# Kernel tuning notes

Measured on AMD Instinct MI355X. Metric: run time of the kernel, lower is better.

The kernel has to match this reference:

```python
import jax, jax.numpy as jnp
import numpy as np

DIM, DEPTH, MULT = 512, 3, 4
E = 2 ** DEPTH            # 8 experts
HID = MULT * DIM          # 2048
B, S = 4, 1024


def setup_inputs() -> dict:
    key = jax.random.key(0)
    ks = jax.random.split(key, 7)
    sd = 1.0 / np.sqrt(DIM)
    sh = 1.0 / np.sqrt(HID)
    return {
        "x": jax.random.normal(ks[0], (B, S, DIM), dtype=jnp.float32),
        "rw": jax.random.normal(ks[1], (E - 1, DIM), dtype=jnp.float32) * sd,
        "rb": jax.random.normal(ks[2], (E - 1,), dtype=jnp.float32) * sd,
        "w1": jax.random.normal(ks[3], (E, DIM, HID), dtype=jnp.float32) * sd,
        "b1": jax.random.normal(ks[4], (E, HID), dtype=jnp.float32) * sd,
        "w2": jax.random.normal(ks[5], (E, HID, DIM), dtype=jnp.float32) * sh,
        "b2": jax.random.normal(ks[6], (E, DIM), dtype=jnp.float32) * sh,
    }


def _leaf_probs(flat_x, rw, rb):
    # Binary-tree soft routing: level d has 2**d routers at offset 2**d - 1.
    n_tok = flat_x.shape[0]
    leaf = jnp.ones((n_tok, 1), dtype=flat_x.dtype)
    for d in range(DEPTH):
        off, n = 2 ** d - 1, 2 ** d
        logits = flat_x @ rw[off:off + n].T + rb[off:off + n]   # [N, n]
        p = jax.nn.sigmoid(logits)
        # child probs: left = 1-p, right = p
        leaf = (leaf[:, :, None] * jnp.stack([1.0 - p, p], axis=2)).reshape(n_tok, 2 * n)
    return leaf  # [N, E]


def reference(x, rw, rb, w1, b1, w2, b2):
    b, s, dim = x.shape
    flat_x = x.reshape(b * s, dim)                               # [N, D]
    leaf_probs = _leaf_probs(flat_x, rw, rb)                     # [N, E]
    # Dense evaluation of all experts (soft-routing training path).
    h = jnp.einsum('nd,edh->neh', flat_x, w1) + b1[None]         # [N, E, H]
    h = jax.nn.gelu(h, approximate=False)                        # torch nn.GELU (erf)
    y = jnp.einsum('neh,ehd->ned', h, w2) + b2[None]             # [N, E, D]
    out = jnp.einsum('ned,ne->nd', y, leaf_probs)                # [N, D]
    return out.reshape(b, s, dim)
```

## Files before the change

kernel.cpp:

```cpp
#include <hip/hip_runtime.h>
#include <hip/hip_bf16.h>
#include <hip/hip_fp16.h>

#define DIM 512
#define HID 2048
#define NE 8
#define NTOK 4096

typedef _Float16 v8h __attribute__((ext_vector_type(8)));
typedef float v16f __attribute__((ext_vector_type(16)));

__device__ __forceinline__ void load16(const void* g, void* l) {
  __builtin_amdgcn_global_load_lds(
      (const __attribute__((address_space(1))) unsigned int*)g,
      (__attribute__((address_space(3))) unsigned int*)l, 16, 0, 0);
}

__device__ __forceinline__ float gelu_fast(float v) {
  float v2 = v * v;
  float u = v * __builtin_fmaf(0.07135481627f, v2, 1.5957691216f);
  float t = __expf(-u);
  return v * __builtin_amdgcn_rcpf(1.0f + t);
}

__global__ __launch_bounds__(256) void pre_kernel(const float* __restrict__ x,
                                                  const float* __restrict__ rw,
                                                  const float* __restrict__ rb,
                                                  const float* __restrict__ b2,
                                                  const float* __restrict__ w1,
                                                  const float* __restrict__ w2,
                                                  float* __restrict__ leaf,
                                                  _Float16* __restrict__ xh,
                                                  float* __restrict__ out,
                                                  _Float16* __restrict__ w1t,
                                                  _Float16* __restrict__ w2t) {
  __shared__ float tile[32][65];
  if (blockIdx.x < 1024) {
    const int lane = threadIdx.x & 63;
    const int wave = threadIdx.x >> 6;
    const int n = (blockIdx.x << 2) + wave;
    const float4* xv = (const float4*)(x + (size_t)n * DIM);
    const float4 x0 = xv[lane * 2], x1 = xv[lane * 2 + 1];
    v8h o;
    o[0] = (_Float16)x0.x; o[1] = (_Float16)x0.y; o[2] = (_Float16)x0.z; o[3] = (_Float16)x0.w;
    o[4] = (_Float16)x1.x; o[5] = (_Float16)x1.y; o[6] = (_Float16)x1.z; o[7] = (_Float16)x1.w;
    *(v8h*)(xh + (size_t)n * DIM + lane * 8) = o;
    float logits[7];
#pragma unroll
    for (int rr = 0; rr < 7; ++rr) {
      const float4* wv = (const float4*)(rw + rr * DIM);
      const float4 w0 = wv[lane * 2], w1v = wv[lane * 2 + 1];
      float s = x0.x * w0.x + x0.y * w0.y + x0.z * w0.z + x0.w * w0.w +
                x1.x * w1v.x + x1.y * w1v.y + x1.z * w1v.z + x1.w * w1v.w;
#pragma unroll
      for (int o2 = 32; o2; o2 >>= 1) s += __shfl_xor(s, o2, 64);
      logits[rr] = s + rb[rr];
    }
    const int eidx = lane & 7;
    const float p0 = 1.f / (1.f + __expf(-logits[0]));
    float f = ((eidx >> 2) & 1) ? p0 : 1.f - p0;
    const float p1 = 1.f / (1.f + __expf(-logits[1 + (eidx >> 2)]));
    f *= ((eidx >> 1) & 1) ? p1 : 1.f - p1;
    const float p2 = 1.f / (1.f + __expf(-logits[3 + (eidx >> 1)]));
    f *= (eidx & 1) ? p2 : 1.f - p2;
    if (lane < NE) leaf[(size_t)n * NE + lane] = f;
    float le[NE];
#pragma unroll
    for (int e = 0; e < NE; ++e) le[e] = __shfl(f, e, 64);
    float4 a0 = {0.f, 0.f, 0.f, 0.f}, a1 = {0.f, 0.f, 0.f, 0.f};
#pragma unroll
    for (int e = 0; e < NE; ++e) {
      const float4* bv = (const float4*)(b2 + (size_t)e * DIM + lane * 8);
      const float4 u0 = bv[0], u1 = bv[1];
      a0.x += le[e] * u0.x; a0.y += le[e] * u0.y; a0.z += le[e] * u0.z; a0.w += le[e] * u0.w;
      a1.x += le[e] * u1.x; a1.y += le[e] * u1.y; a1.z += le[e] * u1.z; a1.w += le[e] * u1.w;
    }
    float4* op = (float4*)(out + (size_t)n * DIM + lane * 8);
    op[0] = a0; op[1] = a1;
  } else {
    int bx = blockIdx.x - 1024;
    const float* in;
    _Float16* outp;
    int R, C;
    if (bx < 4096) { in = w1; outp = w1t; R = DIM; C = HID; }
    else { bx -= 4096; in = w2; outp = w2t; R = HID; C = DIM; }
    const int e = bx >> 9;
    const int rem = bx & 511;
    const int tiles_r = R >> 6;
    const int rt = rem % tiles_r;
    const int ct = rem / tiles_r;
    const int r0 = rt << 6, c0 = ct << 5;
    const size_t ebase = (size_t)e * R * C;
    const int tid = threadIdx.x;
#pragma unroll
    for (int it = 0; it < 2; ++it) {
      const int s = tid + (it << 8);
      const int row = s >> 3, cq = s & 7;
      const float4 v = *(const float4*)(in + ebase + (size_t)(r0 + row) * C + c0 + (cq << 2));
      tile[(cq << 2) + 0][row] = v.x;
      tile[(cq << 2) + 1][row] = v.y;
      tile[(cq << 2) + 2][row] = v.z;
      tile[(cq << 2) + 3][row] = v.w;
    }
    __syncthreads();
    const int c = tid >> 3, seg = tid & 7;
    v8h hv;
#pragma unroll
    for (int u = 0; u < 8; ++u) hv[u] = (_Float16)tile[c][(seg << 3) + u];
    *(v8h*)(outp + ebase + (size_t)(c0 + c) * R + r0 + (seg << 3)) = hv;
  }
}

__global__ __launch_bounds__(256, 2) void gemm1_kernel(const _Float16* __restrict__ xh,
                                                       const _Float16* __restrict__ w1t,
                                                       const float* __restrict__ b1,
                                                       const float* __restrict__ leaf,
                                                       _Float16* __restrict__ H) {
  const int bx = blockIdx.x;
  const int e = bx & 7;
  const int t = bx >> 3;
  const int mt = t & 15;
  const int nt = t >> 4;
  const int m0 = mt << 8, n0 = nt << 7;

  __shared__ alignas(16) _Float16 As[256 * 64];
  __shared__ alignas(16) _Float16 Bs[128 * 64];

  const int tid = threadIdx.x;
  const int lane = tid & 63;
  const int wave = tid >> 6;
  const int wm = wave >> 1, wn = wave & 1;
  const int c = lane & 31, h2 = lane >> 5;
  const int cx = c & 7;

  const int strow = tid >> 3;
  const int c8 = (tid & 7) ^ (strow & 7);
  const _Float16* pa[8];
  const _Float16* pb[4];
  _Float16* la[8];
  _Float16* lb[4];
#pragma unroll
  for (int i = 0; i < 8; ++i) {
    pa[i] = xh + (size_t)(m0 + strow + 32 * i) * DIM + (c8 << 3);
    la[i] = As + tid * 8 + i * 2048;
  }
#pragma unroll
  for (int i = 0; i < 4; ++i) {
    pb[i] = w1t + ((size_t)e * HID + n0 + strow + 32 * i) * DIM + (c8 << 3);
    lb[i] = Bs + tid * 8 + i * 2048;
  }
  const _Float16* fA[4];
  const _Float16* fB[2];
#pragma unroll
  for (int i = 0; i < 4; ++i) fA[i] = As + ((wm << 7) + (i << 5) + c) * 64;
#pragma unroll
  for (int j = 0; j < 2; ++j) fB[j] = Bs + ((wn << 6) + (j << 5) + c) * 64;

  v16f acc[4][2];
#pragma unroll
  for (int i = 0; i < 4; ++i)
#pragma unroll
    for (int j = 0; j < 2; ++j)
      acc[i][j] = v16f{0.f,0.f,0.f,0.f,0.f,0.f,0.f,0.f,0.f,0.f,0.f,0.f,0.f,0.f,0.f,0.f};

#pragma unroll
  for (int kk = 0; kk < 8; ++kk) {
#pragma unroll
    for (int i = 0; i < 8; ++i) load16(pa[i] + kk * 64, la[i]);
#pragma unroll
    for (int i = 0; i < 4; ++i) load16(pb[i] + kk * 64, lb[i]);
    __syncthreads();
#pragma unroll
    for (int ks = 0; ks < 4; ++ks) {
      const int so = ((((ks << 1) + h2) ^ cx) << 3);
      v8h a[4], b[2];
#pragma unroll
      for (int i = 0; i < 4; ++i) a[i] = *(const v8h*)(fA[i] + so);
#pragma unroll
      for (int j = 0; j < 2; ++j) b[j] = *(const v8h*)(fB[j] + so);
#pragma unroll
      for (int i = 0; i < 4; ++i)
#pragma unroll
        for (int j = 0; j < 2; ++j)
          acc[i][j] = __builtin_amdgcn_mfma_f32_32x32x16_f16(a[i], b[j], acc[i][j], 0, 0, 0);
    }
    __syncthreads();
  }

  const float* b1e = b1 + (size_t)e * HID;
  _Float16* He = H + (size_t)e * NTOK * HID;
  const int colb = n0 + (wn << 6) + c;
  const float bias0 = b1e[colb];
  const float bias1 = b1e[colb + 32];
#pragma unroll
  for (int i = 0; i < 4; ++i) {
    const int rb0 = m0 + (wm << 7) + (i << 5) + (h2 << 2);
#pragma unroll
    for (int rg = 0; rg < 4; ++rg) {
#pragma unroll
      for (int rr = 0; rr < 4; ++rr) {
        const int row = rb0 + (rg << 3) + rr;
        const int reg = (rg << 2) + rr;
        const float p = leaf[(size_t)row * NE + e];
        _Float16* hp = He + (size_t)row * HID + colb;
        hp[0]  = (_Float16)(p * gelu_fast(acc[i][0][reg] + bias0));
        hp[32] = (_Float16)(p * gelu_fast(acc[i][1][reg] + bias1));
      }
    }
  }
}

__global__ __launch_bounds__(256, 2) void gemm2_kernel(const _Float16* __restrict__ H,
                                                       const _Float16* __restrict__ w2t,
                                                       float* __restrict__ out) {
  const int bx = blockIdx.x;
  const int e = bx & 7;
  const int dt = (bx >> 3) & 3;
  const int mt = bx >> 5;
  const int m0 = mt << 8, d0 = dt << 7;

  __shared__ alignas(16) _Float16 As[256 * 64];
  __shared__ alignas(16) _Float16 Bs[128 * 64];

  const int tid = threadIdx.x;
  const int lane = tid & 63;
  const int wave = tid >> 6;
  const int wm = wave >> 1, wn = wave & 1;
  const int c = lane & 31, h2 = lane >> 5;
  const int cx = c & 7;

  const int strow = tid >> 3;
  const int c8 = (tid & 7) ^ (strow & 7);
  const _Float16* pa[8];
  const _Float16* pb[4];
  _Float16* la[8];
  _Float16* lb[4];
#pragma unroll
  for (int i = 0; i < 8; ++i) {
    pa[i] = H + ((size_t)e * NTOK + m0 + strow + 32 * i) * HID + (c8 << 3);
    la[i] = As + tid * 8 + i * 2048;
  }
#pragma unroll
  for (int i = 0; i < 4; ++i) {
    pb[i] = w2t + ((size_t)e * DIM + d0 + strow + 32 * i) * HID + (c8 << 3);
    lb[i] = Bs + tid * 8 + i * 2048;
  }
  const _Float16* fA[4];
  const _Float16* fB[2];
#pragma unroll
  for (int i = 0; i < 4; ++i) fA[i] = As + ((wm << 7) + (i << 5) + c) * 64;
#pragma unroll
  for (int j = 0; j < 2; ++j) fB[j] = Bs + ((wn << 6) + (j << 5) + c) * 64;

  v16f acc[4][2];
#pragma unroll
  for (int i = 0; i < 4; ++i)
#pragma unroll
    for (int j = 0; j < 2; ++j)
      acc[i][j] = v16f{0.f,0.f,0.f,0.f,0.f,0.f,0.f,0.f,0.f,0.f,0.f,0.f,0.f,0.f,0.f,0.f};

  for (int ko = 0; ko < 4; ++ko) {
#pragma unroll
    for (int u = 0; u < 8; ++u) {
#pragma unroll
      for (int i = 0; i < 8; ++i) load16(pa[i] + u * 64, la[i]);
#pragma unroll
      for (int i = 0; i < 4; ++i) load16(pb[i] + u * 64, lb[i]);
      __syncthreads();
#pragma unroll
      for (int ks = 0; ks < 4; ++ks) {
        const int so = ((((ks << 1) + h2) ^ cx) << 3);
        v8h a[4], b[2];
#pragma unroll
        for (int i = 0; i < 4; ++i) a[i] = *(const v8h*)(fA[i] + so);
#pragma unroll
        for (int j = 0; j < 2; ++j) b[j] = *(const v8h*)(fB[j] + so);
#pragma unroll
        for (int i = 0; i < 4; ++i)
#pragma unroll
          for (int j = 0; j < 2; ++j)
            acc[i][j] = __builtin_amdgcn_mfma_f32_32x32x16_f16(a[i], b[j], acc[i][j], 0, 0, 0);
      }
      __syncthreads();
    }
#pragma unroll
    for (int i = 0; i < 8; ++i) pa[i] += 512;
#pragma unroll
    for (int i = 0; i < 4; ++i) pb[i] += 512;
  }

#pragma unroll
  for (int i = 0; i < 4; ++i) {
    const int rb0 = m0 + (wm << 7) + (i << 5) + (h2 << 2);
#pragma unroll
    for (int rg = 0; rg < 4; ++rg) {
#pragma unroll
      for (int rr = 0; rr < 4; ++rr) {
        const int row = rb0 + (rg << 3) + rr;
        const int reg = (rg << 2) + rr;
        float* op = out + (size_t)row * DIM + d0 + (wn << 6) + c;
        atomicAdd(op, acc[i][0][reg]);
        atomicAdd(op + 32, acc[i][1][reg]);
      }
    }
  }
}

extern "C" void kernel_launch(void* const* d_in, const int* in_sizes, int n_in,
                              void* d_out, int out_size, void* d_ws, size_t ws_size,
                              hipStream_t stream) {
  const float* x  = (const float*)d_in[0];
  const float* rw = (const float*)d_in[1];
  const float* rb = (const float*)d_in[2];
  const float* w1 = (const float*)d_in[3];
  const float* b1 = (const float*)d_in[4];
  const float* w2 = (const float*)d_in[5];
  const float* b2 = (const float*)d_in[6];
  float* out = (float*)d_out;

  char* ws = (char*)d_ws;
  const size_t xh_bytes   = (size_t)NTOK * DIM * 2;
  const size_t w1t_bytes  = (size_t)NE * HID * DIM * 2;
  const size_t w2t_bytes  = (size_t)NE * DIM * HID * 2;
  const size_t leaf_bytes = (size_t)NTOK * NE * 4;
  const size_t H_bytes    = (size_t)NE * NTOK * HID * 2;
  _Float16* xh   = (_Float16*)(ws);
  _Float16* w1t  = (_Float16*)(ws + xh_bytes);
  _Float16* w2t  = (_Float16*)(ws + xh_bytes + w1t_bytes);
  float*    leaf = (float*)(ws + xh_bytes + w1t_bytes + w2t_bytes);
  _Float16* Hbuf = (_Float16*)(ws + xh_bytes + w1t_bytes + w2t_bytes + leaf_bytes);
  if (ws_size < xh_bytes + w1t_bytes + w2t_bytes + leaf_bytes + H_bytes) return;

  pre_kernel<<<9216, 256, 0, stream>>>(x, rw, rb, b2, w1, w2, leaf, xh, out, w1t, w2t);
  gemm1_kernel<<<2048, 256, 0, stream>>>(xh, w1t, b1, leaf, Hbuf);
  gemm2_kernel<<<512, 256, 0, stream>>>(Hbuf, w2t, out);
}
```

Baseline: 328.4 us.

## Enlarge GEMM tiles to 256x256, load B from global into registers, double-buffer A

Both expert GEMMs move from 256x128 tiles with 32x32 MFMA to 256x256 tiles using 16x16x32 MFMA. Each wave now holds an 8x8 grid of accumulators and reads B fragments straight from global memory into registers instead of through LDS. A is double-buffered in LDS so the next k-slice loads while the current one computes, with one barrier per step. The weight-transpose blocks in pre_kernel now handle 64x64 tiles, which cuts the grid sizes. The trade-offs are higher register pressure (launch bounds drop to 1 block per SM), fewer blocks in gemm2 (256) and uncoalesced global B reads.

```diff
diff --git a/kernel.cpp b/kernel.cpp
--- a/kernel.cpp
+++ b/kernel.cpp
@@ -8,7 +8,7 @@
 #define NTOK 4096
 
 typedef _Float16 v8h __attribute__((ext_vector_type(8)));
-typedef float v16f __attribute__((ext_vector_type(16)));
+typedef float v4f __attribute__((ext_vector_type(4)));
 
 __device__ __forceinline__ void load16(const void* g, void* l) {
   __builtin_amdgcn_global_load_lds(
@@ -34,7 +34,7 @@
                                                   float* __restrict__ out,
                                                   _Float16* __restrict__ w1t,
                                                   _Float16* __restrict__ w2t) {
-  __shared__ float tile[32][65];
+  __shared__ float tile[64][65];
   if (blockIdx.x < 1024) {
     const int lane = threadIdx.x & 63;
     const int wave = threadIdx.x >> 6;
@@ -78,40 +78,49 @@
     float4* op = (float4*)(out + (size_t)n * DIM + lane * 8);
     op[0] = a0; op[1] = a1;
   } else {
-    int bx = blockIdx.x - 1024;
     const float* in;
     _Float16* outp;
-    int R, C;
-    if (bx < 4096) { in = w1; outp = w1t; R = DIM; C = HID; }
-    else { bx -= 4096; in = w2; outp = w2t; R = HID; C = DIM; }
-    const int e = bx >> 9;
-    const int rem = bx & 511;
-    const int tiles_r = R >> 6;
-    const int rt = rem % tiles_r;
-    const int ct = rem / tiles_r;
-    const int r0 = rt << 6, c0 = ct << 5;
+    int R, C, rt, ct, e;
+    if (blockIdx.x < 3072) {
+      const int bx = blockIdx.x - 1024;
+      in = w1; outp = w1t; R = DIM; C = HID;
+      e = bx >> 8;
+      const int rem = bx & 255;
+      rt = rem & 7; ct = rem >> 3;
+    } else {
+      const int bx = blockIdx.x - 3072;
+      in = w2; outp = w2t; R = HID; C = DIM;
+      e = bx >> 8;
+      const int rem = bx & 255;
+      rt = rem & 31; ct = rem >> 5;
+    }
+    const int r0 = rt << 6, c0 = ct << 6;
     const size_t ebase = (size_t)e * R * C;
     const int tid = threadIdx.x;
 #pragma unroll
+    for (int it = 0; it < 4; ++it) {
+      const int s = tid + (it << 8);
+      const int row = s >> 4, c4 = (s & 15) << 2;
+      const float4 v = *(const float4*)(in + ebase + (size_t)(r0 + row) * C + c0 + c4);
+      tile[c4 + 0][row] = v.x;
+      tile[c4 + 1][row] = v.y;
+      tile[c4 + 2][row] = v.z;
+      tile[c4 + 3][row] = v.w;
+    }
+    __syncthreads();
+#pragma unroll
     for (int it = 0; it < 2; ++it) {
       const int s = tid + (it << 8);
-      const int row = s >> 3, cq = s & 7;
-      const float4 v = *(const float4*)(in + ebase + (size_t)(r0 + row) * C + c0 + (cq << 2));
-      tile[(cq << 2) + 0][row] = v.x;
-      tile[(cq << 2) + 1][row] = v.y;
-      tile[(cq << 2) + 2][row] = v.z;
-      tile[(cq << 2) + 3][row] = v.w;
-    }
-    __syncthreads();
-    const int c = tid >> 3, seg = tid & 7;
-    v8h hv;
-#pragma unroll
-    for (int u = 0; u < 8; ++u) hv[u] = (_Float16)tile[c][(seg << 3) + u];
-    *(v8h*)(outp + ebase + (size_t)(c0 + c) * R + r0 + (seg << 3)) = hv;
-  }
-}
-
-__global__ __launch_bounds__(256, 2) void gemm1_kernel(const _Float16* __restrict__ xh,
+      const int oc = s >> 3, seg = s & 7;
+      v8h hv;
+#pragma unroll
+      for (int u = 0; u < 8; ++u) hv[u] = (_Float16)tile[oc][(seg << 3) + u];
+      *(v8h*)(outp + ebase + (size_t)(c0 + oc) * R + r0 + (seg << 3)) = hv;
+    }
+  }
+}
+
+__global__ __launch_bounds__(256, 1) void gemm1_kernel(const _Float16* __restrict__ xh,
                                                        const _Float16* __restrict__ w1t,
                                                        const float* __restrict__ b1,
                                                        const float* __restrict__ leaf,
@@ -121,187 +130,185 @@
   const int t = bx >> 3;
   const int mt = t & 15;
   const int nt = t >> 4;
-  const int m0 = mt << 8, n0 = nt << 7;
-
-  __shared__ alignas(16) _Float16 As[256 * 64];
-  __shared__ alignas(16) _Float16 Bs[128 * 64];
+  const int m0 = mt << 8, n0 = nt << 8;
+
+  __shared__ alignas(16) _Float16 As[2 * 16384];
 
   const int tid = threadIdx.x;
   const int lane = tid & 63;
   const int wave = tid >> 6;
   const int wm = wave >> 1, wn = wave & 1;
-  const int c = lane & 31, h2 = lane >> 5;
-  const int cx = c & 7;
+  const int r = lane & 15, q = lane >> 4;
 
   const int strow = tid >> 3;
   const int c8 = (tid & 7) ^ (strow & 7);
   const _Float16* pa[8];
-  const _Float16* pb[4];
   _Float16* la[8];
-  _Float16* lb[4];
 #pragma unroll
   for (int i = 0; i < 8; ++i) {
     pa[i] = xh + (size_t)(m0 + strow + 32 * i) * DIM + (c8 << 3);
     la[i] = As + tid * 8 + i * 2048;
   }
-#pragma unroll
-  for (int i = 0; i < 4; ++i) {
-    pb[i] = w1t + ((size_t)e * HID + n0 + strow + 32 * i) * DIM + (c8 << 3);
-    lb[i] = Bs + tid * 8 + i * 2048;
-  }
-  const _Float16* fA[4];
-  const _Float16* fB[2];
-#pragma unroll
-  for (int i = 0; i < 4; ++i) fA[i] = As + ((wm << 7) + (i << 5) + c) * 64;
-#pragma unroll
-  for (int j = 0; j < 2; ++j) fB[j] = Bs + ((wn << 6) + (j << 5) + c) * 64;
-
-  v16f acc[4][2];
-#pragma unroll
-  for (int i = 0; i < 4; ++i)
-#pragma unroll
-    for (int j = 0; j < 2; ++j)
-      acc[i][j] = v16f{0.f,0.f,0.f,0.f,0.f,0.f,0.f,0.f,0.f,0.f,0.f,0.f,0.f,0.f,0.f,0.f};
+  int aoff[8];
+#pragma unroll
+  for (int i = 0; i < 8; ++i)
+    aoff[i] = (((wm << 7) + (i << 4) + r) << 6) + ((q ^ (r & 7)) << 3);
+  const _Float16* pb[8];
+#pragma unroll
+  for (int j = 0; j < 8; ++j)
+    pb[j] = w1t + ((size_t)e * HID + n0 + (wn << 7) + (j << 4) + r) * DIM + (q << 3);
+
+  v4f acc[8][8];
+#pragma unroll
+  for (int i = 0; i < 8; ++i)
+#pragma unroll
+    for (int j = 0; j < 8; ++j) acc[i][j] = v4f{0.f, 0.f, 0.f, 0.f};
+
+#pragma unroll
+  for (int i = 0; i < 8; ++i) load16(pa[i], la[i]);
 
 #pragma unroll
   for (int kk = 0; kk < 8; ++kk) {
-#pragma unroll
-    for (int i = 0; i < 8; ++i) load16(pa[i] + kk * 64, la[i]);
-#pragma unroll
-    for (int i = 0; i < 4; ++i) load16(pb[i] + kk * 64, lb[i]);
     __syncthreads();
-#pragma unroll
-    for (int ks = 0; ks < 4; ++ks) {
-      const int so = ((((ks << 1) + h2) ^ cx) << 3);
-      v8h a[4], b[2];
-#pragma unroll
-      for (int i = 0; i < 4; ++i) a[i] = *(const v8h*)(fA[i] + so);
-#pragma unroll
-      for (int j = 0; j < 2; ++j) b[j] = *(const v8h*)(fB[j] + so);
-#pragma unroll
-      for (int i = 0; i < 4; ++i)
-#pragma unroll
-        for (int j = 0; j < 2; ++j)
-          acc[i][j] = __builtin_amdgcn_mfma_f32_32x32x16_f16(a[i], b[j], acc[i][j], 0, 0, 0);
-    }
-    __syncthreads();
+    v8h b0[8], b1v[8];
+#pragma unroll
+    for (int j = 0; j < 8; ++j) b0[j] = *(const v8h*)(pb[j] + kk * 64);
+#pragma unroll
+    for (int j = 0; j < 8; ++j) b1v[j] = *(const v8h*)(pb[j] + kk * 64 + 32);
+    if (kk < 7) {
+      const int off = (((kk + 1) & 1) << 14);
+#pragma unroll
+      for (int i = 0; i < 8; ++i) load16(pa[i] + (kk + 1) * 64, la[i] + off);
+    }
+    const int cp = (kk & 1) << 14;
+    v8h a0[8];
+#pragma unroll
+    for (int i = 0; i < 8; ++i) a0[i] = *(const v8h*)(As + cp + aoff[i]);
+#pragma unroll
+    for (int i = 0; i < 8; ++i)
+#pragma unroll
+      for (int j = 0; j < 8; ++j)
+        acc[i][j] = __builtin_amdgcn_mfma_f32_16x16x32_f16(a0[i], b0[j], acc[i][j], 0, 0, 0);
+#pragma unroll
+    for (int i = 0; i < 8; ++i) a0[i] = *(const v8h*)(As + cp + (aoff[i] ^ 32));
+#pragma unroll
+    for (int i = 0; i < 8; ++i)
+#pragma unroll
+      for (int j = 0; j < 8; ++j)
+        acc[i][j] = __builtin_amdgcn_mfma_f32_16x16x32_f16(a0[i], b1v[j], acc[i][j], 0, 0, 0);
   }
 
   const float* b1e = b1 + (size_t)e * HID;
   _Float16* He = H + (size_t)e * NTOK * HID;
-  const int colb = n0 + (wn << 6) + c;
-  const float bias0 = b1e[colb];
-  const float bias1 = b1e[colb + 32];
-#pragma unroll
-  for (int i = 0; i < 4; ++i) {
-    const int rb0 = m0 + (wm << 7) + (i << 5) + (h2 << 2);
-#pragma unroll
-    for (int rg = 0; rg < 4; ++rg) {
-#pragma unroll
-      for (int rr = 0; rr < 4; ++rr) {
-        const int row = rb0 + (rg << 3) + rr;
-        const int reg = (rg << 2) + rr;
-        const float p = leaf[(size_t)row * NE + e];
-        _Float16* hp = He + (size_t)row * HID + colb;
-        hp[0]  = (_Float16)(p * gelu_fast(acc[i][0][reg] + bias0));
-        hp[32] = (_Float16)(p * gelu_fast(acc[i][1][reg] + bias1));
-      }
-    }
-  }
-}
-
-__global__ __launch_bounds__(256, 2) void gemm2_kernel(const _Float16* __restrict__ H,
+  float bias[8];
+#pragma unroll
+  for (int j = 0; j < 8; ++j) bias[j] = b1e[n0 + (wn << 7) + (j << 4) + r];
+#pragma unroll
+  for (int i = 0; i < 8; ++i) {
+    const int rowb = m0 + (wm << 7) + (i << 4) + (q << 2);
+#pragma unroll
+    for (int rr = 0; rr < 4; ++rr) {
+      const int row = rowb + rr;
+      const float p = leaf[(size_t)row * NE + e];
+      _Float16* hp = He + (size_t)row * HID + n0 + (wn << 7) + r;
+#pragma unroll
+      for (int j = 0; j < 8; ++j)
+        hp[j << 4] = (_Float16)(p * gelu_fast(acc[i][j][rr] + bias[j]));
+    }
+  }
+}
+
+__global__ __launch_bounds__(256, 1) void gemm2_kernel(const _Float16* __restrict__ H,
                                                        const _Float16* __restrict__ w2t,
                                                        float* __restrict__ out) {
   const int bx = blockIdx.x;
   const int e = bx & 7;
-  const int dt = (bx >> 3) & 3;
-  const int mt = bx >> 5;
-  const int m0 = mt << 8, d0 = dt << 7;
-
-  __shared__ alignas(16) _Float16 As[256 * 64];
-  __shared__ alignas(16) _Float16 Bs[128 * 64];
+  const int t = bx >> 3;
+  const int nt = t & 1;
+  const int mt = t >> 1;
+  const int m0 = mt << 8, d0 = nt << 8;
+
+  __shared__ alignas(16) _Float16 As[2 * 16384];
 
   const int tid = threadIdx.x;
   const int lane = tid & 63;
   const int wave = tid >> 6;
   const int wm = wave >> 1, wn = wave & 1;
-  const int c = lane & 31, h2 = lane >> 5;
-  const int cx = c & 7;
+  const int r = lane & 15, q = lane >> 4;
 
   const int strow = tid >> 3;
   const int c8 = (tid & 7) ^ (strow & 7);
   const _Float16* pa[8];
-  const _Float16* pb[4];
   _Float16* la[8];
-  _Float16* lb[4];
 #pragma unroll
   for (int i = 0; i < 8; ++i) {
     pa[i] = H + ((size_t)e * NTOK + m0 + strow + 32 * i) * HID + (c8 << 3);
     la[i] = As + tid * 8 + i * 2048;
   }
-#pragma unroll
-  for (int i = 0; i < 4; ++i) {
-    pb[i] = w2t + ((size_t)e * DIM + d0 + strow + 32 * i) * HID + (c8 << 3);
-    lb[i] = Bs + tid * 8 + i * 2048;
-  }
-  const _Float16* fA[4];
-  const _Float16* fB[2];
-#pragma unroll
-  for (int i = 0; i < 4; ++i) fA[i] = As + ((wm << 7) + (i << 5) + c) * 64;
-#pragma unroll
-  for (int j = 0; j < 2; ++j) fB[j] = Bs + ((wn << 6) + (j << 5) + c) * 64;
-
-  v16f acc[4][2];
-#pragma unroll
-  for (int i = 0; i < 4; ++i)
-#pragma unroll
-    for (int j = 0; j < 2; ++j)
-      acc[i][j] = v16f{0.f,0.f,0.f,0.f,0.f,0.f,0.f,0.f,0.f,0.f,0.f,0.f,0.f,0.f,0.f,0.f};
+  int aoff[8];
+#pragma unroll
+  for (int i = 0; i < 8; ++i)
+    aoff[i] = (((wm << 7) + (i << 4) + r) << 6) + ((q ^ (r & 7)) << 3);
+  const _Float16* pb[8];
+#pragma unroll
+  for (int j = 0; j < 8; ++j)
+    pb[j] = w2t + ((size_t)e * DIM + d0 + (wn << 7) + (j << 4) + r) * HID + (q << 3);
+
+  v4f acc[8][8];
+#pragma unroll
+  for (int i = 0; i < 8; ++i)
+#pragma unroll
+    for (int j = 0; j < 8; ++j) acc[i][j] = v4f{0.f, 0.f, 0.f, 0.f};
+
+#pragma unroll
+  for (int i = 0; i < 8; ++i) load16(pa[i], la[i]);
 
   for (int ko = 0; ko < 4; ++ko) {
 #pragma unroll
     for (int u = 0; u < 8; ++u) {
-#pragma unroll
-      for (int i = 0; i < 8; ++i) load16(pa[i] + u * 64, la[i]);
-#pragma unroll
-      for (int i = 0; i < 4; ++i) load16(pb[i] + u * 64, lb[i]);
       __syncthreads();
-#pragma unroll
-      for (int ks = 0; ks < 4; ++ks) {
-        const int so = ((((ks << 1) + h2) ^ cx) << 3);
-        v8h a[4], b[2];
-#pragma unroll
-        for (int i = 0; i < 4; ++i) a[i] = *(const v8h*)(fA[i] + so);
-#pragma unroll
-        for (int j = 0; j < 2; ++j) b[j] = *(const v8h*)(fB[j] + so);
-#pragma unroll
-        for (int i = 0; i < 4; ++i)
-#pragma unroll
-          for (int j = 0; j < 2; ++j)
-            acc[i][j] = __builtin_amdgcn_mfma_f32_32x32x16_f16(a[i], b[j], acc[i][j], 0, 0, 0);
+      v8h b0[8], b1v[8];
+#pragma unroll
+      for (int j = 0; j < 8; ++j) b0[j] = *(const v8h*)(pb[j] + u * 64);
+#pragma unroll
+      for (int j = 0; j < 8; ++j) b1v[j] = *(const v8h*)(pb[j] + u * 64 + 32);
+      if (!(ko == 3 && u == 7)) {
+        const int off = (((u + 1) & 1) << 14);
+#pragma unroll
+        for (int i = 0; i < 8; ++i) load16(pa[i] + (u + 1) * 64, la[i] + off);
       }
-      __syncthreads();
+      const int cp = (u & 1) << 14;
+      v8h a0[8];
+#pragma unroll
+      for (int i = 0; i < 8; ++i) a0[i] = *(const v8h*)(As + cp + aoff[i]);
+#pragma unroll
+      for (int i = 0; i < 8; ++i)
+#pragma unroll
+        for (int j = 0; j < 8; ++j)
+          acc[i][j] = __builtin_amdgcn_mfma_f32_16x16x32_f16(a0[i], b0[j], acc[i][j], 0, 0, 0);
+#pragma unroll
+      for (int i = 0; i < 8; ++i) a0[i] = *(const v8h*)(As + cp + (aoff[i] ^ 32));
+#pragma unroll
+      for (int i = 0; i < 8; ++i)
+#pragma unroll
+        for (int j = 0; j < 8; ++j)
+          acc[i][j] = __builtin_amdgcn_mfma_f32_16x16x32_f16(a0[i], b1v[j], acc[i][j], 0, 0, 0);
     }
 #pragma unroll
     for (int i = 0; i < 8; ++i) pa[i] += 512;
 #pragma unroll
-    for (int i = 0; i < 4; ++i) pb[i] += 512;
-  }
-
-#pragma unroll
-  for (int i = 0; i < 4; ++i) {
-    const int rb0 = m0 + (wm << 7) + (i << 5) + (h2 << 2);
-#pragma unroll
-    for (int rg = 0; rg < 4; ++rg) {
-#pragma unroll
-      for (int rr = 0; rr < 4; ++rr) {
-        const int row = rb0 + (rg << 3) + rr;
-        const int reg = (rg << 2) + rr;
-        float* op = out + (size_t)row * DIM + d0 + (wn << 6) + c;
-        atomicAdd(op, acc[i][0][reg]);
-        atomicAdd(op + 32, acc[i][1][reg]);
-      }
+    for (int j = 0; j < 8; ++j) pb[j] += 512;
+  }
+
+#pragma unroll
+  for (int i = 0; i < 8; ++i) {
+    const int rowb = m0 + (wm << 7) + (i << 4) + (q << 2);
+#pragma unroll
+    for (int rr = 0; rr < 4; ++rr) {
+      float* op = out + (size_t)(rowb + rr) * DIM + d0 + (wn << 7) + r;
+#pragma unroll
+      for (int j = 0; j < 8; ++j)
+        atomicAdd(op + (j << 4), acc[i][j][rr]);
     }
   }
 }
@@ -331,7 +338,7 @@
   _Float16* Hbuf = (_Float16*)(ws + xh_bytes + w1t_bytes + w2t_bytes + leaf_bytes);
   if (ws_size < xh_bytes + w1t_bytes + w2t_bytes + leaf_bytes + H_bytes) return;
 
-  pre_kernel<<<9216, 256, 0, stream>>>(x, rw, rb, b2, w1, w2, leaf, xh, out, w1t, w2t);
-  gemm1_kernel<<<2048, 256, 0, stream>>>(xh, w1t, b1, leaf, Hbuf);
-  gemm2_kernel<<<512, 256, 0, stream>>>(Hbuf, w2t, out);
-}
+  pre_kernel<<<5120, 256, 0, stream>>>(x, rw, rb, b2, w1, w2, leaf, xh, out, w1t, w2t);
+  gemm1_kernel<<<1024, 256, 0, stream>>>(xh, w1t, b1, leaf, Hbuf);
+  gemm2_kernel<<<256, 256, 0, stream>>>(Hbuf, w2t, out);
+}
```

After: 451.1 us. 1.37x slower.
